# Performance work log

Measured on AMD Instinct MI355X. Metric: run time of the kernel, lower is better.

## Reference

```python
import jax, jax.numpy as jnp
import numpy as np

N_HEAD, D_MODEL, D_K, D_V = 16, 1024, 64, 64
BIAS_WEIGHT = 1.0
NEG = -10000.0


def setup_inputs() -> dict:
    key = jax.random.key(0)
    ks = jax.random.split(key, 9)
    B, L = 2, 2048
    q = jax.random.normal(ks[0], (B, L, D_MODEL), dtype=jnp.float32)
    k = jax.random.normal(ks[1], (B, L, D_MODEL), dtype=jnp.float32)
    v = jax.random.normal(ks[2], (B, L, D_MODEL), dtype=jnp.float32)
    mask = jax.random.randint(ks[3], (B, L, L), 0, 2, dtype=jnp.int32)
    bias = jax.random.normal(ks[4], (B, L, L), dtype=jnp.float32)
    s = 1.0 / np.sqrt(D_MODEL)
    w_qs = jax.random.uniform(ks[5], (D_MODEL, N_HEAD * D_K), jnp.float32, -s, s)
    w_ks = jax.random.uniform(ks[6], (D_MODEL, N_HEAD * D_K), jnp.float32, -s, s)
    w_vs = jax.random.uniform(ks[7], (D_MODEL, N_HEAD * D_V), jnp.float32, -s, s)
    w_fc = jax.random.uniform(ks[8], (N_HEAD * D_V, D_MODEL), jnp.float32, -s, s)
    return {"q": q, "k": k, "v": v, "mask": mask, "bias": bias,
            "w_qs": w_qs, "w_ks": w_ks, "w_vs": w_vs, "w_fc": w_fc}


def reference(q, k, v, mask, bias, w_qs, w_ks, w_vs, w_fc):
    B, Lq, _ = q.shape
    # project and split heads: [B, H, L, d]
    qh = (q @ w_qs).reshape(B, Lq, N_HEAD, D_K).transpose(0, 2, 1, 3)
    kh = (k @ w_ks).reshape(B, k.shape[1], N_HEAD, D_K).transpose(0, 2, 1, 3)
    vh = (v @ w_vs).reshape(B, v.shape[1], N_HEAD, D_V).transpose(0, 2, 1, 3)
    temperature = D_K ** 0.5
    attn = jnp.einsum('bhqd,bhkd->bhqk', qh / temperature, kh)
    attn = attn + bias[:, None, :, :] * BIAS_WEIGHT
    attn = jnp.where(mask[:, None, :, :] == 0, NEG, attn)
    attn = jax.nn.softmax(attn, axis=-1)
    out = jnp.einsum('bhqk,bhkd->bhqd', attn, vh)
    out = out.transpose(0, 2, 1, 3).reshape(B, Lq, N_HEAD * D_V)
    return out @ w_fc
```

## Files before the change

kernel.cpp:

```cpp
#include <hip/hip_runtime.h>
#include <cstddef>

#define DEV static __device__ __forceinline__

typedef float f32x4 __attribute__((ext_vector_type(4)));
typedef __bf16 bf16x8 __attribute__((ext_vector_type(8)));
typedef __bf16 bf16x4v __attribute__((ext_vector_type(4)));
typedef unsigned short u16x8 __attribute__((ext_vector_type(8)));
typedef unsigned short u16x4 __attribute__((ext_vector_type(4)));
typedef _Float16 f16;
typedef _Float16 f16x4 __attribute__((ext_vector_type(4)));

constexpr int BB = 2, LL = 2048, DM = 1024, NH = 16, DK = 64;
constexpr float LOG2E = 1.44269504f;

DEV unsigned short f2bf(float f) {
  unsigned u = __builtin_bit_cast(unsigned, f);
  u += 0x7fffu + ((u >> 16) & 1u);
  return (unsigned short)(u >> 16);
}
DEV u16x4 cvt4(f32x4 v) {
  bf16x4v b = __builtin_convertvector(v, bf16x4v);
  return __builtin_bit_cast(u16x4, b);
}
DEV bf16x8 asbf(u16x8 v) { return __builtin_bit_cast(bf16x8, v); }
DEV f32x4 mfma16(u16x8 a, u16x8 b, f32x4 c) {
  return __builtin_amdgcn_mfma_f32_16x16x32_bf16(asbf(a), asbf(b), c, 0, 0, 0);
}
#if __has_builtin(__builtin_amdgcn_exp2f)
DEV float fexp2(float x) { return __builtin_amdgcn_exp2f(x); }
#else
DEV float fexp2(float x) { return exp2f(x); }
#endif
DEV void g2lds16(const void* g, void* l) {
  __builtin_amdgcn_global_load_lds(
      (const __attribute__((address_space(1))) unsigned int*)g,
      (__attribute__((address_space(3))) unsigned int*)l, 16, 0, 0);
}

__global__ __launch_bounds__(256) void prep_w(const float* __restrict__ w0,
                                              const float* __restrict__ w1,
                                              const float* __restrict__ w2,
                                              const float* __restrict__ w3,
                                              unsigned short* __restrict__ wT) {
  __shared__ float tile[32][33];
  int z = blockIdx.z;
  const float* W = (z == 0) ? w0 : (z == 1) ? w1 : (z == 2) ? w2 : w3;
  unsigned short* out = wT + (size_t)z * DM * DM;
  int k0 = blockIdx.y * 32, n0 = blockIdx.x * 32;
  int tx = threadIdx.x, ty = threadIdx.y;
#pragma unroll
  for (int p = 0; p < 4; p++)
    tile[ty + 8 * p][tx] = W[(size_t)(k0 + ty + 8 * p) * DM + n0 + tx];
  __syncthreads();
#pragma unroll
  for (int p = 0; p < 4; p++)
    out[(size_t)(n0 + ty + 8 * p) * DM + k0 + tx] = f2bf(tile[tx][ty + 8 * p]);
}

__global__ __launch_bounds__(256) void prep_bm(const int* __restrict__ mask,
                                               const float* __restrict__ bias,
                                               f16* __restrict__ bm) {
  size_t i = ((size_t)blockIdx.x * 256 + threadIdx.x) * 4;
  int4 mk = *(const int4*)(mask + i);
  float4 bs = *(const float4*)(bias + i);
  f16x4 o;
  o[0] = (f16)((mk.x == 0 ? -10000.f : bs.x) * LOG2E);
  o[1] = (f16)((mk.y == 0 ? -10000.f : bs.y) * LOG2E);
  o[2] = (f16)((mk.z == 0 ? -10000.f : bs.z) * LOG2E);
  o[3] = (f16)((mk.w == 0 ? -10000.f : bs.w) * LOG2E);
  *(f16x4*)(bm + i) = o;
}

__global__ __launch_bounds__(256) void prep_cvt(const float* __restrict__ s0,
                                                const float* __restrict__ s1,
                                                const float* __restrict__ s2,
                                                unsigned short* __restrict__ dst) {
  int z = blockIdx.y;
  const float* src = (z == 0) ? s0 : (z == 1) ? s1 : s2;
  size_t i = ((size_t)blockIdx.x * 256 + threadIdx.x) * 8;
  float4 a = *(const float4*)(src + i);
  float4 b = *(const float4*)(src + i + 4);
  u16x8 o;
  o[0] = f2bf(a.x); o[1] = f2bf(a.y); o[2] = f2bf(a.z); o[3] = f2bf(a.w);
  o[4] = f2bf(b.x); o[5] = f2bf(b.y); o[6] = f2bf(b.z); o[7] = f2bf(b.w);
  *(u16x8*)(dst + (size_t)z * (size_t)(BB * LL) * DM + i) = o;
}

template <int KITERS>
DEV void gemm_core(const unsigned short* __restrict__ A,
                   const unsigned short* __restrict__ BT,
                   unsigned short (*Al)[128 * 64], unsigned short (*Bl)[128 * 64],
                   int m0, int n0, int k0beg, int t, f32x4 (&acc)[4][4]) {
  int lane = t & 63, c = lane & 15, qd = lane >> 4;
  int w = t >> 6, wm = w >> 1, wn = w & 1;
  int r0 = t >> 3;
  int gsw = (t & 7) ^ (r0 & 7);
  u16x8 ar[4], br[4];

  auto load_tile = [&](int k0) {
#pragma unroll
    for (int p = 0; p < 4; ++p) {
      ar[p] = *(const u16x8*)&A[(size_t)(m0 + 32 * p + r0) * DM + k0 + 8 * gsw];
      br[p] = *(const u16x8*)&BT[(size_t)(n0 + 32 * p + r0) * DM + k0 + 8 * gsw];
    }
  };
  auto store_tile = [&](int buf) {
#pragma unroll
    for (int p = 0; p < 4; ++p) {
      *(u16x8*)&Al[buf][p * 2048 + t * 8] = ar[p];
      *(u16x8*)&Bl[buf][p * 2048 + t * 8] = br[p];
    }
  };
  auto compute = [&](int buf) {
#pragma unroll
    for (int ks = 0; ks < 2; ++ks) {
      u16x8 af[4], bfr[4];
#pragma unroll
      for (int mt = 0; mt < 4; ++mt)
        af[mt] = *(const u16x8*)&Al[buf][(64 * wm + 16 * mt + c) * 64 +
                                         (((4 * ks + qd) ^ (c & 7)) << 3)];
#pragma unroll
      for (int nt = 0; nt < 4; ++nt)
        bfr[nt] = *(const u16x8*)&Bl[buf][(64 * wn + 16 * nt + c) * 64 +
                                          (((4 * ks + qd) ^ (c & 7)) << 3)];
#pragma unroll
      for (int mt = 0; mt < 4; ++mt)
#pragma unroll
        for (int nt = 0; nt < 4; ++nt)
          acc[mt][nt] = mfma16(af[mt], bfr[nt], acc[mt][nt]);
    }
  };

  load_tile(k0beg);
  store_tile(0);
  __syncthreads();
#pragma unroll 1
  for (int kk = 0; kk < KITERS; ++kk) {
    if (kk + 1 < KITERS) load_tile(k0beg + (kk + 1) * 64);
    compute(kk & 1);
    if (kk + 1 < KITERS) store_tile((kk + 1) & 1);
    __syncthreads();
  }
}

__global__ __launch_bounds__(256) void proj_gemm(const unsigned short* __restrict__ qkvb,
                                                 const unsigned short* __restrict__ wT,
                                                 unsigned short* __restrict__ qh,
                                                 unsigned short* __restrict__ kh,
                                                 unsigned short* __restrict__ vT) {
  __shared__ unsigned short Al[2][128 * 64];
  __shared__ unsigned short Bl[2][128 * 64];
  int z = blockIdx.z;
  const unsigned short* A = qkvb + (size_t)z * BB * LL * DM;
  const unsigned short* BT = wT + (size_t)z * DM * DM;
  int t = threadIdx.x, lane = t & 63, c = lane & 15, qd = lane >> 4;
  int w = t >> 6, wm = w >> 1, wn = w & 1;
  int m0 = blockIdx.y * 128, n0 = blockIdx.x * 128;
  f32x4 acc[4][4] = {};
  gemm_core<DM / 64>(A, BT, Al, Bl, m0, n0, 0, t, acc);

  if (z == 2) {
#pragma unroll
    for (int mt = 0; mt < 4; ++mt)
#pragma unroll
      for (int nt = 0; nt < 4; ++nt) {
        int n = n0 + 64 * wn + 16 * nt + c;
        int h = n >> 6, d = n & 63;
        int m = m0 + 64 * wm + 16 * mt + 4 * qd;
        int b = m >> 11, l = m & 2047;
        *(u16x4*)&vT[(((size_t)b * NH + h) * DK + d) * LL + l] = cvt4(acc[mt][nt]);
      }
  } else {
    unsigned short* Ch = z ? kh : qh;
    float scale = z ? 1.0f : 0.125f * LOG2E;
#pragma unroll
    for (int mt = 0; mt < 4; ++mt)
#pragma unroll
      for (int nt = 0; nt < 4; ++nt) {
        int n = n0 + 64 * wn + 16 * nt + c;
        int h = n >> 6, d = n & 63;
#pragma unroll
        for (int i = 0; i < 4; ++i) {
          int m = m0 + 64 * wm + 16 * mt + 4 * qd + i;
          int b = m >> 11, l = m & 2047;
          Ch[(((size_t)b * NH + h) * LL + l) * DK + d] = f2bf(acc[mt][nt][i] * scale);
        }
      }
  }
}

__global__ __launch_bounds__(256) void fc_gemm(const unsigned short* __restrict__ A,
                                               const unsigned short* __restrict__ BT,
                                               float* __restrict__ C) {
  __shared__ unsigned short Al[2][128 * 64];
  __shared__ unsigned short Bl[2][128 * 64];
  int t = threadIdx.x, lane = t & 63, c = lane & 15, qd = lane >> 4;
  int w = t >> 6, wm = w >> 1, wn = w & 1;
  int m0 = blockIdx.y * 128, n0 = blockIdx.x * 128;
  f32x4 acc[4][4] = {};
  gemm_core<8>(A, BT, Al, Bl, m0, n0, blockIdx.z * 512, t, acc);
#pragma unroll
  for (int mt = 0; mt < 4; ++mt)
#pragma unroll
    for (int nt = 0; nt < 4; ++nt) {
      int n = n0 + 64 * wn + 16 * nt + c;
#pragma unroll
      for (int i = 0; i < 4; ++i) {
        int m = m0 + 64 * wm + 16 * mt + 4 * qd + i;
        unsafeAtomicAdd(&C[(size_t)m * DM + n], acc[mt][nt][i]);
      }
    }
}

__global__ __launch_bounds__(256) void attn_kern(const unsigned short* __restrict__ qh,
                                                 const unsigned short* __restrict__ kh,
                                                 const unsigned short* __restrict__ vT,
                                                 const f16* __restrict__ bm,
                                                 unsigned short* __restrict__ O) {
  __shared__ unsigned short Kb[2][4096];
  __shared__ unsigned short Vb[2][4096];
  __shared__ f16 Bb[2][8192];
  __shared__ unsigned short Pq[4][32][64];
  unsigned short* Ql = &Pq[0][0][0];

  int t = threadIdx.x, w = t >> 6, lane = t & 63, c = lane & 15, qd = lane >> 4;
  int q0 = blockIdx.x * 128, h = blockIdx.y, b = blockIdx.z;
  const unsigned short* Q = qh + (((size_t)b * NH + h) * LL + q0) * DK;
  const unsigned short* K = kh + ((size_t)b * NH + h) * LL * DK;
  const unsigned short* V = vT + ((size_t)b * NH + h) * DK * LL;
  const f16* BM = bm + ((size_t)b * LL + q0) * LL;
  int rt = t >> 3, gg = t & 7;

#pragma unroll
  for (int r = 0; r < 4; ++r) {
    int row = r * 32 + rt;
    int sc = ((gg ^ (row & 7)) << 3);
    g2lds16(&Q[(size_t)row * DK + sc], &Ql[r * 2048 + w * 512]);
    g2lds16(&BM[(size_t)row * LL + sc], &Bb[0][r * 2048 + w * 512]);
  }
#pragma unroll
  for (int r = 0; r < 2; ++r) {
    int row = r * 32 + rt;
    int sc = ((gg ^ (row & 7)) << 3);
    g2lds16(&K[(size_t)row * DK + sc], &Kb[0][r * 2048 + w * 512]);
    g2lds16(&V[(size_t)row * LL + sc], &Vb[0][r * 2048 + w * 512]);
  }
  __syncthreads();
  u16x8 qf[2][2];
#pragma unroll
  for (int nt = 0; nt < 2; ++nt)
#pragma unroll
    for (int ks = 0; ks < 2; ++ks)
      qf[nt][ks] = *(const u16x8*)&Ql[(32 * w + 16 * nt + c) * 64 +
                                      (((4 * ks + qd) ^ (c & 7)) << 3)];
  __syncthreads();

  float li[2] = {0.f, 0.f};
  f32x4 oacc[4][2] = {};

#pragma unroll 1
  for (int it = 0; it < 32; ++it) {
    int cur = it & 1;
    const unsigned short* Kl = Kb[cur];
    const unsigned short* Vt = Vb[cur];
    if (it + 1 < 32) {
      int nb = cur ^ 1, kt1 = (it + 1) * 64;
#pragma unroll
      for (int r = 0; r < 2; ++r) {
        int row = r * 32 + rt;
        int sc = ((gg ^ (row & 7)) << 3);
        g2lds16(&K[(size_t)(kt1 + row) * DK + sc], &Kb[nb][r * 2048 + w * 512]);
        g2lds16(&V[(size_t)row * LL + kt1 + sc], &Vb[nb][r * 2048 + w * 512]);
      }
#pragma unroll
      for (int r = 0; r < 4; ++r) {
        int row = r * 32 + rt;
        int sc = ((gg ^ (row & 7)) << 3);
        g2lds16(&BM[(size_t)row * LL + kt1 + sc], &Bb[nb][r * 2048 + w * 512]);
      }
    }

    f32x4 s[4][2];
#pragma unroll
    for (int mt = 0; mt < 4; ++mt) {
      int row = 16 * mt + c;
      u16x8 k0f = *(const u16x8*)&Kl[row * 64 + ((qd ^ (c & 7)) << 3)];
      u16x8 k1f = *(const u16x8*)&Kl[row * 64 + (((4 + qd) ^ (c & 7)) << 3)];
#pragma unroll
      for (int nt = 0; nt < 2; ++nt) {
        f32x4 z = {0.f, 0.f, 0.f, 0.f};
        z = mfma16(k0f, qf[nt][0], z);
        s[mt][nt] = mfma16(k1f, qf[nt][1], z);
      }
    }
#pragma unroll
    for (int nt = 0; nt < 2; ++nt) {
      int qrow = (32 * w + 16 * nt + c) * 64;
#pragma unroll
      for (int mt = 0; mt < 4; ++mt) {
        f16x4 b4 = *(const f16x4*)&Bb[cur][qrow +
                                           (((2 * mt + (qd >> 1)) ^ (c & 7)) << 3) +
                                           ((qd & 1) << 2)];
        f32x4 p;
#pragma unroll
        for (int i = 0; i < 4; ++i) {
          p[i] = fexp2(s[mt][nt][i] + (float)b4[i]);
          li[nt] += p[i];
        }
        int off = (((2 * mt + (qd >> 1)) ^ (c & 7)) << 3) + ((qd & 1) << 2);
        *(u16x4*)&Pq[w][16 * nt + c][off] = cvt4(p);
      }
    }
    u16x8 pf[2][2];
#pragma unroll
    for (int nt = 0; nt < 2; ++nt)
#pragma unroll
      for (int ks = 0; ks < 2; ++ks)
        pf[nt][ks] =
            *(const u16x8*)&Pq[w][16 * nt + c][(((4 * ks + qd) ^ (c & 7)) << 3)];
#pragma unroll
    for (int dt = 0; dt < 4; ++dt) {
      int row = 16 * dt + c;
      u16x8 v0f = *(const u16x8*)&Vt[row * 64 + ((qd ^ (c & 7)) << 3)];
      u16x8 v1f = *(const u16x8*)&Vt[row * 64 + (((4 + qd) ^ (c & 7)) << 3)];
#pragma unroll
      for (int nt = 0; nt < 2; ++nt) {
        oacc[dt][nt] = mfma16(v0f, pf[nt][0], oacc[dt][nt]);
        oacc[dt][nt] = mfma16(v1f, pf[nt][1], oacc[dt][nt]);
      }
    }
    __syncthreads();
  }

#pragma unroll
  for (int nt = 0; nt < 2; ++nt) {
    float l = li[nt];
    l += __shfl_xor(l, 16);
    l += __shfl_xor(l, 32);
    float rl = 1.f / l;
    size_t orow = ((size_t)b * LL + q0 + 32 * w + 16 * nt + c) * DM + h * DK;
#pragma unroll
    for (int dt = 0; dt < 4; ++dt)
      *(u16x4*)&O[orow + 16 * dt + 4 * qd] = cvt4(oacc[dt][nt] * rl);
  }
}

extern "C" void kernel_launch(void* const* d_in, const int* in_sizes, int n_in,
                              void* d_out, int out_size, void* d_ws, size_t ws_size,
                              hipStream_t stream) {
  (void)in_sizes; (void)n_in; (void)ws_size;
  const float* q = (const float*)d_in[0];
  const float* k = (const float*)d_in[1];
  const float* v = (const float*)d_in[2];
  const int* mask = (const int*)d_in[3];
  const float* bias = (const float*)d_in[4];
  const float* w_qs = (const float*)d_in[5];
  const float* w_ks = (const float*)d_in[6];
  const float* w_vs = (const float*)d_in[7];
  const float* w_fc = (const float*)d_in[8];

  char* ws = (char*)d_ws;
  const size_t MB = 1024 * 1024;
  unsigned short* wT = (unsigned short*)(ws);
  f16* bmw = (f16*)(ws + 8 * MB);
  unsigned short* qkvb = (unsigned short*)(ws + 24 * MB);
  unsigned short* qh = (unsigned short*)(ws + 48 * MB);
  unsigned short* kh = (unsigned short*)(ws + 56 * MB);
  unsigned short* vhT = (unsigned short*)(ws + 64 * MB);
  unsigned short* Obuf = (unsigned short*)(ws + 72 * MB);

  prep_w<<<dim3(32, 32, 4), dim3(32, 8, 1), 0, stream>>>(w_qs, w_ks, w_vs, w_fc, wT);
  prep_bm<<<dim3(8192), dim3(256), 0, stream>>>(mask, bias, bmw);
  prep_cvt<<<dim3(2048, 3), dim3(256), 0, stream>>>(q, k, v, qkvb);
  proj_gemm<<<dim3(8, 32, 3), 256, 0, stream>>>(qkvb, wT, qh, kh, vhT);
  attn_kern<<<dim3(16, 16, 2), 256, 0, stream>>>(qh, kh, vhT, bmw, Obuf);
  hipMemsetAsync(d_out, 0, (size_t)out_size * sizeof(float), stream);
  fc_gemm<<<dim3(8, 32, 2), 256, 0, stream>>>(Obuf, wT + (size_t)3 * DM * DM,
                                              (float*)d_out);
}
```

Baseline: 313.1 us.

## Load bias into registers and shuffle P via permlane swaps instead of LDS

The attention kernel now loads the f16 bias/mask tile straight from global memory into registers, double-buffered across iterations, instead of staging it through LDS. The softmax probabilities are rearranged into the MFMA B-operand layout with permlane32/permlane16 swaps instead of an LDS write and read-back. Q is staged temporarily in the second K/V buffers, so the Pq and Bb shared arrays go away. The goal is to cut LDS traffic and footprint, which may allow higher occupancy, at the cost of more registers and uncoalesced 8-byte global bias loads. The loop is unrolled by two to alternate the bias register buffers.

After: 326.0 us. +4.1%, slower.

```diff
diff --git a/kernel.cpp b/kernel.cpp
--- a/kernel.cpp
+++ b/kernel.cpp
@@ -8,6 +8,8 @@
 typedef __bf16 bf16x4v __attribute__((ext_vector_type(4)));
 typedef unsigned short u16x8 __attribute__((ext_vector_type(8)));
 typedef unsigned short u16x4 __attribute__((ext_vector_type(4)));
+typedef unsigned u32x2 __attribute__((ext_vector_type(2)));
+typedef unsigned u32x4 __attribute__((ext_vector_type(4)));
 typedef _Float16 f16;
 typedef _Float16 f16x4 __attribute__((ext_vector_type(4)));
 
@@ -32,6 +34,22 @@
 #else
 DEV float fexp2(float x) { return exp2f(x); }
 #endif
+DEV void swap32(unsigned& a, unsigned& b) {
+#if __has_builtin(__builtin_amdgcn_permlane32_swap)
+  u32x2 r = __builtin_amdgcn_permlane32_swap(a, b, false, false);
+  a = r[0]; b = r[1];
+#else
+  asm("v_permlane32_swap_b32 %0, %1" : "+v"(a), "+v"(b));
+#endif
+}
+DEV void swap16(unsigned& a, unsigned& b) {
+#if __has_builtin(__builtin_amdgcn_permlane16_swap)
+  u32x2 r = __builtin_amdgcn_permlane16_swap(a, b, false, false);
+  a = r[0]; b = r[1];
+#else
+  asm("v_permlane16_swap_b32 %0, %1" : "+v"(a), "+v"(b));
+#endif
+}
 DEV void g2lds16(const void* g, void* l) {
   __builtin_amdgcn_global_load_lds(
       (const __attribute__((address_space(1))) unsigned int*)g,
@@ -220,9 +238,6 @@
                                                  unsigned short* __restrict__ O) {
   __shared__ unsigned short Kb[2][4096];
   __shared__ unsigned short Vb[2][4096];
-  __shared__ f16 Bb[2][8192];
-  __shared__ unsigned short Pq[4][32][64];
-  unsigned short* Ql = &Pq[0][0][0];
 
   int t = threadIdx.x, w = t >> 6, lane = t & 63, c = lane & 15, qd = lane >> 4;
   int q0 = blockIdx.x * 128, h = blockIdx.y, b = blockIdx.z;
@@ -231,13 +246,16 @@
   const unsigned short* V = vT + ((size_t)b * NH + h) * DK * LL;
   const f16* BM = bm + ((size_t)b * LL + q0) * LL;
   int rt = t >> 3, gg = t & 7;
+  const f16* BMr0 = BM + (size_t)(32 * w + c) * LL + 4 * qd;
+  const f16* BMr1 = BMr0 + (size_t)16 * LL;
 
 #pragma unroll
   for (int r = 0; r < 4; ++r) {
     int row = r * 32 + rt;
     int sc = ((gg ^ (row & 7)) << 3);
-    g2lds16(&Q[(size_t)row * DK + sc], &Ql[r * 2048 + w * 512]);
-    g2lds16(&BM[(size_t)row * LL + sc], &Bb[0][r * 2048 + w * 512]);
+    unsigned short* qdst = (r < 2) ? &Kb[1][r * 2048 + w * 512]
+                                   : &Vb[1][(r - 2) * 2048 + w * 512];
+    g2lds16(&Q[(size_t)row * DK + sc], qdst);
   }
 #pragma unroll
   for (int r = 0; r < 2; ++r) {
@@ -246,21 +264,28 @@
     g2lds16(&K[(size_t)row * DK + sc], &Kb[0][r * 2048 + w * 512]);
     g2lds16(&V[(size_t)row * LL + sc], &Vb[0][r * 2048 + w * 512]);
   }
+  f16x4 bA[8], bB[8];
+#pragma unroll
+  for (int nt = 0; nt < 2; ++nt)
+#pragma unroll
+    for (int mt = 0; mt < 4; ++mt)
+      bA[nt * 4 + mt] = *(const f16x4*)((nt ? BMr1 : BMr0) + 16 * mt);
   __syncthreads();
+
   u16x8 qf[2][2];
+  const unsigned short* Qs = (w < 2) ? &Kb[1][0] : &Vb[1][0];
 #pragma unroll
   for (int nt = 0; nt < 2; ++nt)
 #pragma unroll
     for (int ks = 0; ks < 2; ++ks)
-      qf[nt][ks] = *(const u16x8*)&Ql[(32 * w + 16 * nt + c) * 64 +
+      qf[nt][ks] = *(const u16x8*)&Qs[(32 * (w & 1) + 16 * nt + c) * 64 +
                                       (((4 * ks + qd) ^ (c & 7)) << 3)];
   __syncthreads();
 
   float li[2] = {0.f, 0.f};
   f32x4 oacc[4][2] = {};
 
-#pragma unroll 1
-  for (int it = 0; it < 32; ++it) {
+  auto body = [&](int it, f16x4 (&bc)[8], f16x4 (&bn)[8]) {
     int cur = it & 1;
     const unsigned short* Kl = Kb[cur];
     const unsigned short* Vt = Vb[cur];
@@ -274,11 +299,10 @@
         g2lds16(&V[(size_t)row * LL + kt1 + sc], &Vb[nb][r * 2048 + w * 512]);
       }
 #pragma unroll
-      for (int r = 0; r < 4; ++r) {
-        int row = r * 32 + rt;
-        int sc = ((gg ^ (row & 7)) << 3);
-        g2lds16(&BM[(size_t)row * LL + kt1 + sc], &Bb[nb][r * 2048 + w * 512]);
-      }
+      for (int nt = 0; nt < 2; ++nt)
+#pragma unroll
+        for (int mt = 0; mt < 4; ++mt)
+          bn[nt * 4 + mt] = *(const f16x4*)((nt ? BMr1 : BMr0) + kt1 + 16 * mt);
     }
 
     f32x4 s[4][2];
@@ -294,31 +318,33 @@
         s[mt][nt] = mfma16(k1f, qf[nt][1], z);
       }
     }
+    u16x8 pf[2][2];
 #pragma unroll
     for (int nt = 0; nt < 2; ++nt) {
-      int qrow = (32 * w + 16 * nt + c) * 64;
+      unsigned L[4], H[4];
 #pragma unroll
       for (int mt = 0; mt < 4; ++mt) {
-        f16x4 b4 = *(const f16x4*)&Bb[cur][qrow +
-                                           (((2 * mt + (qd >> 1)) ^ (c & 7)) << 3) +
-                                           ((qd & 1) << 2)];
+        f16x4 b4 = bc[nt * 4 + mt];
         f32x4 p;
 #pragma unroll
         for (int i = 0; i < 4; ++i) {
           p[i] = fexp2(s[mt][nt][i] + (float)b4[i]);
           li[nt] += p[i];
         }
-        int off = (((2 * mt + (qd >> 1)) ^ (c & 7)) << 3) + ((qd & 1) << 2);
-        *(u16x4*)&Pq[w][16 * nt + c][off] = cvt4(p);
-      }
-    }
-    u16x8 pf[2][2];
-#pragma unroll
-    for (int nt = 0; nt < 2; ++nt)
-#pragma unroll
-      for (int ks = 0; ks < 2; ++ks)
-        pf[nt][ks] =
-            *(const u16x8*)&Pq[w][16 * nt + c][(((4 * ks + qd) ^ (c & 7)) << 3)];
+        u32x2 lw = __builtin_bit_cast(u32x2, cvt4(p));
+        L[mt] = lw[0];
+        H[mt] = lw[1];
+      }
+#pragma unroll
+      for (int ks = 0; ks < 2; ++ks) {
+        unsigned l0 = L[2 * ks], l1 = L[2 * ks + 1];
+        unsigned h0 = H[2 * ks], h1 = H[2 * ks + 1];
+        swap32(l0, l1); swap16(l0, l1);
+        swap32(h0, h1); swap16(h0, h1);
+        u32x4 pw = {l0, h0, l1, h1};
+        pf[nt][ks] = __builtin_bit_cast(u16x8, pw);
+      }
+    }
 #pragma unroll
     for (int dt = 0; dt < 4; ++dt) {
       int row = 16 * dt + c;
@@ -331,6 +357,12 @@
       }
     }
     __syncthreads();
+  };
+
+#pragma unroll 1
+  for (int it = 0; it < 32; it += 2) {
+    body(it, bA, bB);
+    body(it + 1, bB, bA);
   }
 
 #pragma unroll
```
